# Kernel tuning notes

Measured on AMD Instinct MI355X. Metric: run time of the kernel, lower is better.

Reference implementation:

```python
import jax, jax.numpy as jnp
import numpy as np

N_VERTS = 40962  # icosphere level-6 vertex count
K_RING = 19      # 2-ring filter size


def setup_inputs() -> dict:
    key = jax.random.key(0)
    k1, k2, k3, k4 = jax.random.split(key, 4)
    B, C_in, C_out = 4, 64, 64
    x = jax.random.normal(k1, (B, C_in, N_VERTS), dtype=jnp.float32)
    neigh_orders = jax.random.randint(k2, (N_VERTS, K_RING), 0, N_VERTS, dtype=jnp.int32)
    # nn.Linear(19*in_feats, out_feats): weight [C_out, 19*C_in], bias [C_out]
    fan_in = K_RING * C_in
    bound = 1.0 / np.sqrt(fan_in)
    W = jax.random.uniform(k3, (C_out, fan_in), dtype=jnp.float32, minval=-bound, maxval=bound)
    b = jax.random.uniform(k4, (C_out,), dtype=jnp.float32, minval=-bound, maxval=bound)
    return {"x": x, "neigh_orders": neigh_orders, "W": W, "b": b}


def reference(x, neigh_orders, W, b):
    # x: [B, C_in, N] -> [B, N, C_in]
    xt = jnp.transpose(x, (0, 2, 1))
    B, N, C = xt.shape
    # gather 19-ring neighbors: [B, N, 19, C_in]
    gathered = xt[:, neigh_orders, :]
    # im2col-style flatten: [B, N, 19*C_in]
    mat = gathered.reshape(B, N, K_RING * C)
    # Linear: mat @ W.T + b -> [B, N, C_out]
    out = jnp.einsum('bnk,ok->bno', mat, W) + b
    # back to [B, C_out, N]
    return jnp.transpose(out, (0, 2, 1))
```

## Files before the change

### kernel.cpp

```cpp
#include <hip/hip_runtime.h>
#include <hip/hip_bf16.h>


#define NV   40962
#define KR   19
#define CIN  64
#define COUT 64
#define NB   4
#define NTILES 321

typedef __bf16 bf16;
typedef __bf16 bf16x8 __attribute__((ext_vector_type(8)));
typedef float  floatx4 __attribute__((ext_vector_type(4)));

#define XT_ELEMS ((size_t)NB * NV * CIN)
#define WB_OFF   ((XT_ELEMS * 2 + 255) & ~(size_t)255)
#define WF_BYTES ((size_t)COUT * KR * CIN * 2)
#define P1_OFF   ((WB_OFF + WF_BYTES + 255) & ~(size_t)255)
#define WS_SPLIT (P1_OFF + XT_ELEMS * 2)
#define WS_MID   (WB_OFF + WF_BYTES)

__global__ __launch_bounds__(256) void transpose_kernel(
    const float* __restrict__ x, bf16* __restrict__ xt)
{
    __shared__ float tile[64 * 65];
    const int b  = blockIdx.y;
    const int v0 = blockIdx.x * 64;
    const int t  = threadIdx.x;

    if (v0 + 64 <= NV) {
        #pragma unroll
        for (int r = 0; r < 4; ++r) {
            int flat = r * 256 + t;
            int c    = flat >> 4;
            int v4   = (flat & 15) * 4;
            floatx4 val = *(const floatx4*)&x[((size_t)(b * CIN + c)) * NV + v0 + v4];
            tile[(v4 + 0) * 65 + c] = val.x;
            tile[(v4 + 1) * 65 + c] = val.y;
            tile[(v4 + 2) * 65 + c] = val.z;
            tile[(v4 + 3) * 65 + c] = val.w;
        }
    } else {
        const int vl = t & 63;
        const int c0 = t >> 6;
        const int vg = min(v0 + vl, NV - 1);
        #pragma unroll
        for (int p = 0; p < 16; ++p) {
            int c = c0 * 16 + p;
            tile[vl * 65 + c] = x[((size_t)(b * CIN + c)) * NV + vg];
        }
    }
    __syncthreads();

    const int v = t >> 2;
    const int q = t & 3;
    if (v0 + v < NV) {
        #pragma unroll
        for (int p = 0; p < 2; ++p) {
            int chunk = q + p * 4;
            bf16x8 o;
            #pragma unroll
            for (int j = 0; j < 8; ++j)
                o[j] = (bf16)tile[v * 65 + chunk * 8 + j];
            int kc = chunk >> 2;
            size_t dst = ((size_t)((b * 2 + kc) * NV + v0 + v)) * 32 + (chunk & 3) * 8;
            __builtin_nontemporal_store(o, (bf16x8*)&xt[dst]);
        }
    }
}

__global__ __launch_bounds__(256) void convw_kernel(
    const float* __restrict__ W, bf16* __restrict__ Wf)
{
    const int idx = blockIdx.x * 256 + threadIdx.x;
    if (idx >= 2 * KR * 4 * 64) return;
    const int lane = idx & 63;
    const int ot   = (idx >> 6) & 3;
    const int q    = idx >> 8;
    const int kc   = (q >= KR) ? 1 : 0;
    const int ring = q - kc * KR;
    const int row  = ot * 16 + (lane & 15);
    const int col0 = ring * 64 + kc * 32 + (lane >> 4) * 8;
    const float* src = W + (size_t)row * (KR * CIN) + col0;
    floatx4 a = *(const floatx4*)(src);
    floatx4 c = *(const floatx4*)(src + 4);
    bf16x8 o;
    o[0] = (bf16)a.x; o[1] = (bf16)a.y; o[2] = (bf16)a.z; o[3] = (bf16)a.w;
    o[4] = (bf16)c.x; o[5] = (bf16)c.y; o[6] = (bf16)c.z; o[7] = (bf16)c.w;
    *(bf16x8*)(Wf + (size_t)idx * 8) = o;
}

__global__ __launch_bounds__(256, 3) void conv_split_kernel(
    const int*   __restrict__ neigh,
    const bf16*  __restrict__ xt,
    const bf16*  __restrict__ Wf,
    const float* __restrict__ bias,
    float*       __restrict__ out,
    bf16*        __restrict__ P1)
{
    const int i     = blockIdx.x;
    const int slice = i & 7;
    const int b     = slice >> 1;
    const int kc    = slice & 1;
    const int tile  = i >> 3;

    const int t    = threadIdx.x;
    const int wv   = t >> 6;
    const int lane = t & 63;
    const int l15  = lane & 15;
    const int g    = lane >> 4;

    const int n0 = tile * 128 + wv * 32;
    int nn[2], ib[2];
    #pragma unroll
    for (int s = 0; s < 2; ++s) {
        nn[s] = n0 + s * 16 + l15;
        ib[s] = min(nn[s], NV - 1) * KR;
    }

    const bf16* xb = xt + ((size_t)slice * NV) * 32 + g * 8;
    const bf16* wb = Wf + (size_t)kc * (KR * 2048) + lane * 8;

    floatx4 acc[2][4];
    #pragma unroll
    for (int s = 0; s < 2; ++s)
        #pragma unroll
        for (int o = 0; o < 4; ++o)
            acc[s][o] = (floatx4){0.f, 0.f, 0.f, 0.f};

    int inxt[2], i3rd[2];
    bf16x8 xf[2], xg[2], wf[4];
    #pragma unroll
    for (int s = 0; s < 2; ++s) {
        int v0i = neigh[ib[s] + 0];
        inxt[s] = neigh[ib[s] + 1];
        i3rd[s] = neigh[ib[s] + 2];
        int v = ((unsigned)v0i < (unsigned)NV) ? v0i : 0;
        xf[s] = *(const bf16x8*)(xb + (size_t)v * 32);
    }
    #pragma unroll
    for (int f = 0; f < 4; ++f)
        wf[f] = *(const bf16x8*)(wb + f * 512);
    #pragma unroll
    for (int s = 0; s < 2; ++s) {
        int v = ((unsigned)inxt[s] < (unsigned)NV) ? inxt[s] : 0;
        xg[s] = *(const bf16x8*)(xb + (size_t)v * 32);
    }

    #pragma unroll
    for (int r = 0; r < KR; ++r) {
        int inew[2];
        bf16x8 wg[4], xh[2];

        if (r + 3 < KR) {
            #pragma unroll
            for (int s = 0; s < 2; ++s)
                inew[s] = neigh[ib[s] + r + 3];
        }
        if (r + 1 < KR) {
            const bf16* wr = wb + (size_t)(r + 1) * 2048;
            #pragma unroll
            for (int f = 0; f < 4; ++f)
                wg[f] = *(const bf16x8*)(wr + f * 512);
        }
        if (r + 2 < KR) {
            #pragma unroll
            for (int s = 0; s < 2; ++s) {
                int v = ((unsigned)i3rd[s] < (unsigned)NV) ? i3rd[s] : 0;
                xh[s] = *(const bf16x8*)(xb + (size_t)v * 32);
            }
        }

        __builtin_amdgcn_s_setprio(1);
        #pragma unroll
        for (int ot = 0; ot < 4; ++ot)
            #pragma unroll
            for (int s = 0; s < 2; ++s)
                acc[s][ot] = __builtin_amdgcn_mfma_f32_16x16x32_bf16(
                    wf[ot], xf[s], acc[s][ot], 0, 0, 0);
        __builtin_amdgcn_s_setprio(0);

        if (r + 1 < KR) {
            #pragma unroll
            for (int s = 0; s < 2; ++s) xf[s] = xg[s];
            #pragma unroll
            for (int f = 0; f < 4; ++f) wf[f] = wg[f];
        }
        if (r + 2 < KR) {
            #pragma unroll
            for (int s = 0; s < 2; ++s) { xg[s] = xh[s]; inxt[s] = i3rd[s]; i3rd[s] = (r + 3 < KR) ? inew[s] : 0; }
        }
    }

    if (kc == 0) {
        #pragma unroll
        for (int ot = 0; ot < 4; ++ot) {
            #pragma unroll
            for (int ii = 0; ii < 4; ++ii) {
                const int o = ot * 16 + g * 4 + ii;
                const float bv = bias[o];
                #pragma unroll
                for (int s = 0; s < 2; ++s) {
                    if (nn[s] < NV)
                        __builtin_nontemporal_store(acc[s][ot][ii] + bv,
                            &out[((size_t)(b * COUT + o)) * NV + nn[s]]);
                }
            }
        }
    } else {
        #pragma unroll
        for (int ot = 0; ot < 4; ++ot) {
            #pragma unroll
            for (int ii = 0; ii < 4; ++ii) {
                const int o = ot * 16 + g * 4 + ii;
                #pragma unroll
                for (int s = 0; s < 2; ++s) {
                    if (nn[s] < NV)
                        __builtin_nontemporal_store((bf16)acc[s][ot][ii],
                            &P1[((size_t)(b * COUT + o)) * NV + nn[s]]);
                }
            }
        }
    }
}

__global__ __launch_bounds__(256) void reduce_kernel(
    float* __restrict__ out, const bf16* __restrict__ P1)
{
    const size_t total8 = XT_ELEMS / 8;
    for (size_t j = (size_t)blockIdx.x * 256 + threadIdx.x; j < total8;
         j += (size_t)gridDim.x * 256) {
        bf16x8 p = __builtin_nontemporal_load((const bf16x8*)P1 + j);
        floatx4* op = (floatx4*)out + j * 2;
        floatx4 a = __builtin_nontemporal_load(op);
        floatx4 c = __builtin_nontemporal_load(op + 1);
        a.x += (float)p[0]; a.y += (float)p[1]; a.z += (float)p[2]; a.w += (float)p[3];
        c.x += (float)p[4]; c.y += (float)p[5]; c.z += (float)p[6]; c.w += (float)p[7];
        __builtin_nontemporal_store(a, op);
        __builtin_nontemporal_store(c, op + 1);
    }
}

__global__ __launch_bounds__(256, 3) void conv_nosplit_kernel(
    const int*   __restrict__ neigh,
    const bf16*  __restrict__ xt,
    const bf16*  __restrict__ Wf,
    const float* __restrict__ bias,
    float*       __restrict__ out)
{
    const int i    = blockIdx.x;
    const int b    = (i & 7) >> 1;
    const int tile = (i >> 3) * 2 + (i & 1);
    if (tile >= NTILES) return;

    const int t    = threadIdx.x;
    const int wv   = t >> 6;
    const int lane = t & 63;
    const int l15  = lane & 15;
    const int g    = lane >> 4;

    const int n0 = tile * 128 + wv * 32;
    int nn[2], ib[2];
    #pragma unroll
    for (int s = 0; s < 2; ++s) {
        nn[s] = n0 + s * 16 + l15;
        ib[s] = min(nn[s], NV - 1) * KR;
    }

    const bf16* xb0 = xt + ((size_t)(b * 2 + 0) * NV) * 32 + g * 8;
    const bf16* xb1 = xt + ((size_t)(b * 2 + 1) * NV) * 32 + g * 8;
    const bf16* wb  = Wf + lane * 8;

    floatx4 acc[2][4];
    #pragma unroll
    for (int s = 0; s < 2; ++s)
        #pragma unroll
        for (int o = 0; o < 4; ++o)
            acc[s][o] = (floatx4){0.f, 0.f, 0.f, 0.f};

    int inxt[2];
    bf16x8 xf[2][2], wf[2][4];
    #pragma unroll
    for (int s = 0; s < 2; ++s) {
        int v0i = neigh[ib[s] + 0];
        inxt[s] = neigh[ib[s] + 1];
        int v = ((unsigned)v0i < (unsigned)NV) ? v0i : 0;
        xf[s][0] = *(const bf16x8*)(xb0 + (size_t)v * 32);
        xf[s][1] = *(const bf16x8*)(xb1 + (size_t)v * 32);
    }
    #pragma unroll
    for (int kc = 0; kc < 2; ++kc)
        #pragma unroll
        for (int f = 0; f < 4; ++f)
            wf[kc][f] = *(const bf16x8*)(wb + (size_t)kc * (KR * 2048) + f * 512);

    #pragma unroll
    for (int r = 0; r < KR; ++r) {
        int inew[2];
        bf16x8 wg[2][4], xg[2][2];
        if (r + 2 < KR) {
            #pragma unroll
            for (int s = 0; s < 2; ++s) inew[s] = neigh[ib[s] + r + 2];
        }
        if (r + 1 < KR) {
            #pragma unroll
            for (int kc = 0; kc < 2; ++kc)
                #pragma unroll
                for (int f = 0; f < 4; ++f)
                    wg[kc][f] = *(const bf16x8*)(wb + (size_t)kc * (KR * 2048)
                                                 + (size_t)(r + 1) * 2048 + f * 512);
            #pragma unroll
            for (int s = 0; s < 2; ++s) {
                int v = ((unsigned)inxt[s] < (unsigned)NV) ? inxt[s] : 0;
                xg[s][0] = *(const bf16x8*)(xb0 + (size_t)v * 32);
                xg[s][1] = *(const bf16x8*)(xb1 + (size_t)v * 32);
            }
        }

        __builtin_amdgcn_s_setprio(1);
        #pragma unroll
        for (int kc = 0; kc < 2; ++kc)
            #pragma unroll
            for (int ot = 0; ot < 4; ++ot)
                #pragma unroll
                for (int s = 0; s < 2; ++s)
                    acc[s][ot] = __builtin_amdgcn_mfma_f32_16x16x32_bf16(
                        wf[kc][ot], xf[s][kc], acc[s][ot], 0, 0, 0);
        __builtin_amdgcn_s_setprio(0);

        if (r + 1 < KR) {
            #pragma unroll
            for (int s = 0; s < 2; ++s) {
                xf[s][0] = xg[s][0];
                xf[s][1] = xg[s][1];
                inxt[s]  = (r + 2 < KR) ? inew[s] : 0;
            }
            #pragma unroll
            for (int kc = 0; kc < 2; ++kc)
                #pragma unroll
                for (int f = 0; f < 4; ++f)
                    wf[kc][f] = wg[kc][f];
        }
    }

    #pragma unroll
    for (int ot = 0; ot < 4; ++ot) {
        #pragma unroll
        for (int ii = 0; ii < 4; ++ii) {
            const int o = ot * 16 + g * 4 + ii;
            const float bv = bias[o];
            #pragma unroll
            for (int s = 0; s < 2; ++s) {
                if (nn[s] < NV)
                    out[((size_t)(b * COUT + o)) * NV + nn[s]] = acc[s][ot][ii] + bv;
            }
        }
    }
}

__global__ __launch_bounds__(64) void fallback_kernel(
    const int*   __restrict__ neigh,
    const float* __restrict__ x,
    const float* __restrict__ W,
    const float* __restrict__ bias,
    float*       __restrict__ out)
{
    __shared__ float xg[KR * CIN];
    const int bn = blockIdx.x;
    const int b  = bn / NV;
    const int n  = bn % NV;
    const int t  = threadIdx.x;

    for (int k = t; k < KR * CIN; k += 64) {
        int r = k / CIN, c = k - r * CIN;
        int v = neigh[n * KR + r];
        v = ((unsigned)v < (unsigned)NV) ? v : 0;
        xg[k] = x[((size_t)(b * CIN + c)) * NV + v];
    }
    __syncthreads();

    float s = bias[t];
    const float* wrow = W + (size_t)t * (KR * CIN);
    for (int k = 0; k < KR * CIN; ++k) s += xg[k] * wrow[k];
    out[((size_t)(b * COUT + t)) * NV + n] = s;
}

extern "C" void kernel_launch(void* const* d_in, const int* in_sizes, int n_in,
                              void* d_out, int out_size, void* d_ws, size_t ws_size,
                              hipStream_t stream)
{
    const float* x     = (const float*)d_in[0];
    const int*   neigh = (const int*)d_in[1];
    const float* W     = (const float*)d_in[2];
    const float* bias  = (const float*)d_in[3];
    float* out = (float*)d_out;

    if (d_ws != nullptr && ws_size >= WS_MID) {
        bf16* xt = (bf16*)d_ws;
        bf16* Wf = (bf16*)((char*)d_ws + WB_OFF);

        dim3 tgrid((NV + 63) / 64, NB);
        transpose_kernel<<<tgrid, 256, 0, stream>>>(x, xt);
        convw_kernel<<<(2 * KR * 4 * 64 + 255) / 256, 256, 0, stream>>>(W, Wf);

        if (ws_size >= WS_SPLIT) {
            bf16* P1 = (bf16*)((char*)d_ws + P1_OFF);
            conv_split_kernel<<<8 * NTILES, 256, 0, stream>>>(
                neigh, xt, Wf, bias, out, P1);
            reduce_kernel<<<2048, 256, 0, stream>>>(out, P1);
        } else {
            int nblk = 8 * ((NTILES + 1) / 2);
            conv_nosplit_kernel<<<nblk, 256, 0, stream>>>(neigh, xt, Wf, bias, out);
        }
    } else {
        fallback_kernel<<<NB * NV, 64, 0, stream>>>(neigh, x, W, bias, out);
    }
}
```

Baseline: 193.8 us.

## Stage conv weights in LDS, merge prep kernels, use nontemporal gathers

```diff
diff --git a/kernel.cpp b/kernel.cpp
--- a/kernel.cpp
+++ b/kernel.cpp
@@ -8,6 +8,7 @@
 #define COUT 64
 #define NB   4
 #define NTILES 321
+#define TBLK 641
 
 typedef __bf16 bf16;
 typedef __bf16 bf16x8 __attribute__((ext_vector_type(8)));
@@ -20,77 +21,79 @@
 #define WS_SPLIT (P1_OFF + XT_ELEMS * 2)
 #define WS_MID   (WB_OFF + WF_BYTES)
 
-__global__ __launch_bounds__(256) void transpose_kernel(
-    const float* __restrict__ x, bf16* __restrict__ xt)
+__global__ __launch_bounds__(256) void prep_kernel(
+    const float* __restrict__ x, const float* __restrict__ W,
+    bf16* __restrict__ xt, bf16* __restrict__ Wf)
 {
     __shared__ float tile[64 * 65];
-    const int b  = blockIdx.y;
-    const int v0 = blockIdx.x * 64;
-    const int t  = threadIdx.x;
-
-    if (v0 + 64 <= NV) {
-        #pragma unroll
-        for (int r = 0; r < 4; ++r) {
-            int flat = r * 256 + t;
-            int c    = flat >> 4;
-            int v4   = (flat & 15) * 4;
-            floatx4 val = *(const floatx4*)&x[((size_t)(b * CIN + c)) * NV + v0 + v4];
-            tile[(v4 + 0) * 65 + c] = val.x;
-            tile[(v4 + 1) * 65 + c] = val.y;
-            tile[(v4 + 2) * 65 + c] = val.z;
-            tile[(v4 + 3) * 65 + c] = val.w;
+    const int bid = blockIdx.x;
+    const int t   = threadIdx.x;
+
+    if (bid < NB * TBLK) {
+        const int b  = bid / TBLK;
+        const int v0 = (bid - b * TBLK) * 64;
+
+        if (v0 + 64 <= NV) {
+            #pragma unroll
+            for (int r = 0; r < 4; ++r) {
+                int flat = r * 256 + t;
+                int c    = flat >> 4;
+                int v4   = (flat & 15) * 4;
+                floatx4 val = *(const floatx4*)&x[((size_t)(b * CIN + c)) * NV + v0 + v4];
+                tile[(v4 + 0) * 65 + c] = val.x;
+                tile[(v4 + 1) * 65 + c] = val.y;
+                tile[(v4 + 2) * 65 + c] = val.z;
+                tile[(v4 + 3) * 65 + c] = val.w;
+            }
+        } else {
+            const int vl = t & 63;
+            const int c0 = t >> 6;
+            const int vg = min(v0 + vl, NV - 1);
+            #pragma unroll
+            for (int p = 0; p < 16; ++p) {
+                int c = c0 * 16 + p;
+                tile[vl * 65 + c] = x[((size_t)(b * CIN + c)) * NV + vg];
+            }
+        }
+        __syncthreads();
+
+        const int v = t >> 2;
+        const int q = t & 3;
+        if (v0 + v < NV) {
+            #pragma unroll
+            for (int p = 0; p < 2; ++p) {
+                int chunk = q + p * 4;
+                bf16x8 o;
+                #pragma unroll
+                for (int j = 0; j < 8; ++j)
+                    o[j] = (bf16)tile[v * 65 + chunk * 8 + j];
+                int kc = chunk >> 2;
+                size_t dst = ((size_t)((b * 2 + kc) * NV + v0 + v)) * 32 + (chunk & 3) * 8;
+                __builtin_nontemporal_store(o, (bf16x8*)&xt[dst]);
+            }
         }
     } else {
-        const int vl = t & 63;
-        const int c0 = t >> 6;
-        const int vg = min(v0 + vl, NV - 1);
-        #pragma unroll
-        for (int p = 0; p < 16; ++p) {
-            int c = c0 * 16 + p;
-            tile[vl * 65 + c] = x[((size_t)(b * CIN + c)) * NV + vg];
-        }
-    }
-    __syncthreads();
-
-    const int v = t >> 2;
-    const int q = t & 3;
-    if (v0 + v < NV) {
-        #pragma unroll
-        for (int p = 0; p < 2; ++p) {
-            int chunk = q + p * 4;
+        const int idx = (bid - NB * TBLK) * 256 + t;
+        if (idx < 2 * KR * 4 * 64) {
+            const int lane = idx & 63;
+            const int ot   = (idx >> 6) & 3;
+            const int q    = idx >> 8;
+            const int kc   = (q >= KR) ? 1 : 0;
+            const int ring = q - kc * KR;
+            const int row  = ot * 16 + (lane & 15);
+            const int col0 = ring * 64 + kc * 32 + (lane >> 4) * 8;
+            const float* src = W + (size_t)row * (KR * CIN) + col0;
+            floatx4 a = *(const floatx4*)(src);
+            floatx4 c = *(const floatx4*)(src + 4);
             bf16x8 o;
-            #pragma unroll
-            for (int j = 0; j < 8; ++j)
-                o[j] = (bf16)tile[v * 65 + chunk * 8 + j];
-            int kc = chunk >> 2;
-            size_t dst = ((size_t)((b * 2 + kc) * NV + v0 + v)) * 32 + (chunk & 3) * 8;
-            __builtin_nontemporal_store(o, (bf16x8*)&xt[dst]);
-        }
-    }
-}
-
-__global__ __launch_bounds__(256) void convw_kernel(
-    const float* __restrict__ W, bf16* __restrict__ Wf)
-{
-    const int idx = blockIdx.x * 256 + threadIdx.x;
-    if (idx >= 2 * KR * 4 * 64) return;
-    const int lane = idx & 63;
-    const int ot   = (idx >> 6) & 3;
-    const int q    = idx >> 8;
-    const int kc   = (q >= KR) ? 1 : 0;
-    const int ring = q - kc * KR;
-    const int row  = ot * 16 + (lane & 15);
-    const int col0 = ring * 64 + kc * 32 + (lane >> 4) * 8;
-    const float* src = W + (size_t)row * (KR * CIN) + col0;
-    floatx4 a = *(const floatx4*)(src);
-    floatx4 c = *(const floatx4*)(src + 4);
-    bf16x8 o;
-    o[0] = (bf16)a.x; o[1] = (bf16)a.y; o[2] = (bf16)a.z; o[3] = (bf16)a.w;
-    o[4] = (bf16)c.x; o[5] = (bf16)c.y; o[6] = (bf16)c.z; o[7] = (bf16)c.w;
-    *(bf16x8*)(Wf + (size_t)idx * 8) = o;
-}
-
-__global__ __launch_bounds__(256, 3) void conv_split_kernel(
+            o[0] = (bf16)a.x; o[1] = (bf16)a.y; o[2] = (bf16)a.z; o[3] = (bf16)a.w;
+            o[4] = (bf16)c.x; o[5] = (bf16)c.y; o[6] = (bf16)c.z; o[7] = (bf16)c.w;
+            *(bf16x8*)(Wf + (size_t)idx * 8) = o;
+        }
+    }
+}
+
+__global__ __launch_bounds__(256, 2) void conv_split_kernel(
     const int*   __restrict__ neigh,
     const bf16*  __restrict__ xt,
     const bf16*  __restrict__ Wf,
@@ -98,6 +101,8 @@
     float*       __restrict__ out,
     bf16*        __restrict__ P1)
 {
+    __shared__ bf16 Wl[16 * 2048];
+
     const int i     = blockIdx.x;
     const int slice = i & 7;
     const int b     = slice >> 1;
@@ -110,6 +115,14 @@
     const int l15  = lane & 15;
     const int g    = lane >> 4;
 
+    const bf16* wsrc = Wf + (size_t)kc * (KR * 2048);
+
+    #pragma unroll
+    for (int ii = 0; ii < 16; ++ii) {
+        int e = (ii * 256 + t) * 8;
+        *(bf16x8*)&Wl[e] = *(const bf16x8*)&wsrc[e];
+    }
+
     const int n0 = tile * 128 + wv * 32;
     int nn[2], ib[2];
     #pragma unroll
@@ -119,7 +132,6 @@
     }
 
     const bf16* xb = xt + ((size_t)slice * NV) * 32 + g * 8;
-    const bf16* wb = Wf + (size_t)kc * (KR * 2048) + lane * 8;
 
     floatx4 acc[2][4];
     #pragma unroll
@@ -128,47 +140,58 @@
         for (int o = 0; o < 4; ++o)
             acc[s][o] = (floatx4){0.f, 0.f, 0.f, 0.f};
 
+    bf16x8 wtail[3][4];
+    #pragma unroll
+    for (int rr = 0; rr < 3; ++rr)
+        #pragma unroll
+        for (int ot = 0; ot < 4; ++ot)
+            wtail[rr][ot] = *(const bf16x8*)(wsrc + ((16 + rr) * 4 + ot) * 512 + lane * 8);
+
     int inxt[2], i3rd[2];
-    bf16x8 xf[2], xg[2], wf[4];
+    bf16x8 xf[2], xg[2];
     #pragma unroll
     for (int s = 0; s < 2; ++s) {
         int v0i = neigh[ib[s] + 0];
         inxt[s] = neigh[ib[s] + 1];
         i3rd[s] = neigh[ib[s] + 2];
         int v = ((unsigned)v0i < (unsigned)NV) ? v0i : 0;
-        xf[s] = *(const bf16x8*)(xb + (size_t)v * 32);
-    }
-    #pragma unroll
-    for (int f = 0; f < 4; ++f)
-        wf[f] = *(const bf16x8*)(wb + f * 512);
+        xf[s] = __builtin_nontemporal_load((const bf16x8*)(xb + (size_t)v * 32));
+    }
     #pragma unroll
     for (int s = 0; s < 2; ++s) {
         int v = ((unsigned)inxt[s] < (unsigned)NV) ? inxt[s] : 0;
-        xg[s] = *(const bf16x8*)(xb + (size_t)v * 32);
-    }
+        xg[s] = __builtin_nontemporal_load((const bf16x8*)(xb + (size_t)v * 32));
+    }
+
+    __syncthreads();
 
     #pragma unroll
     for (int r = 0; r < KR; ++r) {
         int inew[2];
-        bf16x8 wg[4], xh[2];
+        bf16x8 xh[2];
 
         if (r + 3 < KR) {
             #pragma unroll
             for (int s = 0; s < 2; ++s)
                 inew[s] = neigh[ib[s] + r + 3];
         }
-        if (r + 1 < KR) {
-            const bf16* wr = wb + (size_t)(r + 1) * 2048;
-            #pragma unroll
-            for (int f = 0; f < 4; ++f)
-                wg[f] = *(const bf16x8*)(wr + f * 512);
-        }
         if (r + 2 < KR) {
             #pragma unroll
             for (int s = 0; s < 2; ++s) {
                 int v = ((unsigned)i3rd[s] < (unsigned)NV) ? i3rd[s] : 0;
-                xh[s] = *(const bf16x8*)(xb + (size_t)v * 32);
-            }
+                xh[s] = __builtin_nontemporal_load((const bf16x8*)(xb + (size_t)v * 32));
+            }
+        }
+
+        bf16x8 wf[4];
+        if (r < 16) {
+            #pragma unroll
+            for (int ot = 0; ot < 4; ++ot)
+                wf[ot] = *(const bf16x8*)&Wl[(r * 4 + ot) * 512 + lane * 8];
+        } else {
+            #pragma unroll
+            for (int ot = 0; ot < 4; ++ot)
+                wf[ot] = wtail[r - 16][ot];
         }
 
         __builtin_amdgcn_s_setprio(1);
@@ -183,12 +206,14 @@
         if (r + 1 < KR) {
             #pragma unroll
             for (int s = 0; s < 2; ++s) xf[s] = xg[s];
-            #pragma unroll
-            for (int f = 0; f < 4; ++f) wf[f] = wg[f];
         }
         if (r + 2 < KR) {
             #pragma unroll
-            for (int s = 0; s < 2; ++s) { xg[s] = xh[s]; inxt[s] = i3rd[s]; i3rd[s] = (r + 3 < KR) ? inew[s] : 0; }
+            for (int s = 0; s < 2; ++s) {
+                xg[s] = xh[s];
+                inxt[s] = i3rd[s];
+                i3rd[s] = (r + 3 < KR) ? inew[s] : 0;
+            }
         }
     }
 
@@ -399,9 +424,8 @@
         bf16* xt = (bf16*)d_ws;
         bf16* Wf = (bf16*)((char*)d_ws + WB_OFF);
 
-        dim3 tgrid((NV + 63) / 64, NB);
-        transpose_kernel<<<tgrid, 256, 0, stream>>>(x, xt);
-        convw_kernel<<<(2 * KR * 4 * 64 + 255) / 256, 256, 0, stream>>>(W, Wf);
+        int nprep = NB * TBLK + (2 * KR * 4 * 64 + 255) / 256;
+        prep_kernel<<<nprep, 256, 0, stream>>>(x, W, xt, Wf);
 
         if (ws_size >= WS_SPLIT) {
             bf16* P1 = (bf16*)((char*)d_ws + P1_OFF);
```

Measured after the change: 262.1 us. 1.35x slower.
